# Kernel tuning notes

Hardware: AMD Instinct MI355X
Metric: run time of the kernel (lower is better)

Reference implementation:

```python
import jax, jax.numpy as jnp
import numpy as np

EPS = 1e-12
SMOOTH = 9.0
SGR_STEPS = 3


def l2norm(x, axis=-1):
    return x / jnp.maximum(jnp.linalg.norm(x, axis=axis, keepdims=True), EPS)


def setup_inputs() -> dict:
    key = jax.random.key(0)
    d, s = 1024, 256
    n_img, n_cap, L, n_tok = 64, 64, 32, 197  # 197 -> CLS + 14x14 grid

    def xavier(k, shape):
        lim = float(np.sqrt(6.0 / (shape[-2] + shape[-1])))
        return jax.random.uniform(k, shape, jnp.float32, -lim, lim)

    ks = iter(jax.random.split(key, 32))
    inp = {
        "img_embs": jax.random.normal(next(ks), (n_img, n_tok, d), jnp.float32),
        "cap_embs": jax.random.normal(next(ks), (n_cap, L, d), jnp.float32),
        # constant lengths == max length so the vectorized reference matches
        # the original per-caption loop exactly
        "cap_lens": jnp.full((n_cap,), L, dtype=jnp.int32),
        # visual GlobalSelfAttention
        "vG_Wl": xavier(next(ks), (d, d)), "vG_bl": jnp.zeros((d,), jnp.float32),
        "vG_Wg": xavier(next(ks), (d, d)), "vG_bg": jnp.zeros((d,), jnp.float32),
        "vG_Wc": xavier(next(ks), (d, 1)), "vG_bc": jnp.zeros((1,), jnp.float32),
        # textual GlobalSelfAttention
        "tG_Wl": xavier(next(ks), (d, d)), "tG_bl": jnp.zeros((d,), jnp.float32),
        "tG_Wg": xavier(next(ks), (d, d)), "tG_bg": jnp.zeros((d,), jnp.float32),
        "tG_Wc": xavier(next(ks), (d, 1)), "tG_bc": jnp.zeros((1,), jnp.float32),
        # similarity projections
        "W_loc": xavier(next(ks), (d, s)), "b_loc": jnp.zeros((s,), jnp.float32),
        "W_glo": xavier(next(ks), (d, s)), "b_glo": jnp.zeros((s,), jnp.float32),
        "W_eval": xavier(next(ks), (s, 1)), "b_eval": jnp.zeros((1,), jnp.float32),
        # 3 stacked GraphReasoning layers
        "sgr_Wq": xavier(next(ks), (SGR_STEPS, s, s)), "sgr_bq": jnp.zeros((SGR_STEPS, s), jnp.float32),
        "sgr_Wk": xavier(next(ks), (SGR_STEPS, s, s)), "sgr_bk": jnp.zeros((SGR_STEPS, s), jnp.float32),
        "sgr_Wg": xavier(next(ks), (SGR_STEPS, s, s)), "sgr_bg": jnp.zeros((SGR_STEPS, s), jnp.float32),
    }
    return inp


def global_self_attention(local, raw_global, Wl, bl, Wg, bg, Wc, bc):
    # local: (B, N, d), raw_global: (B, d); dropout is identity at eval
    le = jnp.tanh(local @ Wl + bl)
    ge = jnp.tanh(raw_global @ Wg + bg)
    logits = ((le * ge[:, None, :]) @ Wc + bc)[..., 0]  # (B, N)
    weights = jax.nn.softmax(logits, axis=1)
    global_feat = jnp.sum(weights[..., None] * local, axis=1)
    return l2norm(global_feat, axis=-1)


def scan_attention(query, context, smooth=SMOOTH):
    # query: (B, Nq, d), context: (B, Nc, d)
    attn = jnp.einsum("bcd,bqd->bcq", context, query)
    attn = jax.nn.leaky_relu(attn, negative_slope=0.1)
    attn = l2norm(attn, axis=2)                    # normalize over query dim
    attn = jnp.swapaxes(attn, 1, 2)                # (B, Nq, Nc)
    attn = jax.nn.softmax(attn * smooth, axis=2)   # softmax over context
    weighted = jnp.einsum("bqc,bcd->bqd", attn, context)
    return l2norm(weighted, axis=-1)


def graph_reasoning(sim_emb, Wq, bq, Wk, bk, Wg, bg):
    q = sim_emb @ Wq + bq
    k = sim_emb @ Wk + bk
    edge = jax.nn.softmax(jnp.einsum("bnd,bmd->bnm", q, k), axis=-1)
    sgr = jnp.einsum("bnm,bmd->bnd", edge, sim_emb)
    return jax.nn.relu(sgr @ Wg + bg)


def reference(img_embs, cap_embs, cap_lens,
              vG_Wl, vG_bl, vG_Wg, vG_bg, vG_Wc, vG_bc,
              tG_Wl, tG_bl, tG_Wg, tG_bg, tG_Wc, tG_bc,
              W_loc, b_loc, W_glo, b_glo, W_eval, b_eval,
              sgr_Wq, sgr_bq, sgr_Wk, sgr_bk, sgr_Wg, sgr_bg):
    # 197 tokens -> strip CLS (has_cls_token is True)
    img_tokens = img_embs[:, 1:, :]                      # (n_img, 196, d)
    n_img = img_tokens.shape[0]
    img_avg = img_tokens.mean(axis=1)
    img_global = global_self_attention(img_tokens, img_avg,
                                       vG_Wl, vG_bl, vG_Wg, vG_bg, vG_Wc, vG_bc)

    def per_caption(cap_i):                              # cap_i: (L, d)
        L, d = cap_i.shape
        cap_e = jnp.broadcast_to(cap_i[None], (n_img, L, d))
        cap_avg = jnp.broadcast_to(cap_i.mean(axis=0)[None], (n_img, d))
        cap_global = global_self_attention(cap_e, cap_avg,
                                           tG_Wl, tG_bl, tG_Wg, tG_bg, tG_Wc, tG_bc)
        ctx = scan_attention(cap_e, img_tokens)          # (n_img, L, d)
        sim_loc = l2norm((ctx - cap_e) ** 2 @ W_loc + b_loc, axis=-1)
        sim_glo = l2norm((img_global - cap_global) ** 2 @ W_glo + b_glo, axis=-1)
        sim_emb = jnp.concatenate([sim_glo[:, None, :], sim_loc], axis=1)
        for t in range(SGR_STEPS):
            sim_emb = graph_reasoning(sim_emb, sgr_Wq[t], sgr_bq[t],
                                      sgr_Wk[t], sgr_bk[t], sgr_Wg[t], sgr_bg[t])
        return jax.nn.sigmoid(sim_emb[:, 0, :] @ W_eval + b_eval)[:, 0]  # (n_img,)

    sims = jax.vmap(per_caption)(cap_embs)               # (n_cap, n_img)
    return sims.T                                        # (n_img, n_cap)
```

## Files before the change

kernel.cpp:

```cpp
#include <hip/hip_runtime.h>
#include <hip/hip_bf16.h>
#include <math.h>

#define NI 64
#define NC 64
#define NTOK 197
#define TT 196
#define CL 32
#define DD 1024
#define SS 256
#define NN 33
#define EPSN 1e-12f
#define SMOOTHF 9.0f
#define TP 224

typedef __attribute__((ext_vector_type(8))) short bfrag;
typedef __attribute__((ext_vector_type(4))) float f32x4;
#define MFMA(a, b, c) __builtin_amdgcn_mfma_f32_16x16x32_bf16((a), (b), (c), 0, 0, 0)

#define OFF_ATTNT  0
#define OFF_WTILE  14848
#define OFF_WMAX   23552
#define OFF_NRMS   24064
#define OFF_QN     24192
#define OFF_RNQ    24704
#define OFF_SEA    0
#define OFF_EB     17424
#define OFF_R1     22176
#define OFF_WKQ    29088
#define OFF_VBUF   30112
#define SMEM_BYTES 31392

__device__ __forceinline__ float warp_reduce_sum64(float v) {
#pragma unroll
  for (int m = 32; m > 0; m >>= 1) v += __shfl_xor(v, m, 64);
  return v;
}
__device__ __forceinline__ unsigned short f2b(float f) {
  __hip_bfloat16 h = __float2bfloat16(f);
  return *reinterpret_cast<unsigned short*>(&h);
}
__device__ __forceinline__ float b2f(unsigned short u) {
  union { unsigned int i; float f; } v;
  v.i = ((unsigned int)u) << 16;
  return v.f;
}

__global__ void k_avg(const float* __restrict__ img, const float* __restrict__ cap,
                      float* __restrict__ img_avg, float* __restrict__ cap_avg) {
  int bid = blockIdx.x;
  int tid = threadIdx.x;
  if (bid < NI) {
    int b = bid;
    for (int d = tid; d < DD; d += 256) {
      float acc = 0.f;
      const float* p = img + ((size_t)b * NTOK + 1) * DD + d;
      for (int t = 0; t < TT; ++t) acc += p[(size_t)t * DD];
      img_avg[b * DD + d] = acc * (1.0f / TT);
    }
  } else {
    int c = bid - NI;
    for (int d = tid; d < DD; d += 256) {
      float acc = 0.f;
      const float* p = cap + (size_t)c * CL * DD + d;
      for (int t = 0; t < CL; ++t) acc += p[(size_t)t * DD];
      cap_avg[c * DD + d] = acc * (1.0f / CL);
    }
  }
}

__global__ void k_hvec(const float* __restrict__ avg, const float* __restrict__ Wg,
                       const float* __restrict__ bg, const float* __restrict__ Wc,
                       float* __restrict__ h) {
  __shared__ float av[DD];
  int b = blockIdx.x >> 2;
  int dc = blockIdx.x & 3;
  int tid = threadIdx.x;
  for (int i = tid; i < DD; i += 256) av[i] = avg[b * DD + i];
  __syncthreads();
  int d = dc * 256 + tid;
  float acc = 0.f;
  for (int k = 0; k < DD; k += 4) {
    float4 a4 = *(const float4*)&av[k];
    acc += a4.x * Wg[(size_t)(k + 0) * DD + d];
    acc += a4.y * Wg[(size_t)(k + 1) * DD + d];
    acc += a4.z * Wg[(size_t)(k + 2) * DD + d];
    acc += a4.w * Wg[(size_t)(k + 3) * DD + d];
  }
  h[b * DD + d] = tanhf(acc + bg[d]) * Wc[d];
}

__global__ void k_logits2(const unsigned short* __restrict__ Ai, const unsigned short* __restrict__ Wi,
                          const float* __restrict__ bli, const float* __restrict__ hi,
                          float* __restrict__ pi,
                          const unsigned short* __restrict__ Ac, const unsigned short* __restrict__ Wc2,
                          const float* __restrict__ blc, const float* __restrict__ hc,
                          float* __restrict__ pc) {
  int tid = threadIdx.x;
  int lane = tid & 63, w = tid >> 6;
  int lrow = lane & 15, lk = (lane >> 4) * 8, rsub = (lane >> 4) * 4;
  int bx = blockIdx.x;
  const unsigned short* Abf;
  const unsigned short* WT;
  const float* bl;
  const float* h;
  float* partial;
  int rb, rowsPerBatch;
  if (bx < 196) {
    Abf = Ai; WT = Wi; bl = bli; h = hi; partial = pi; rb = bx * 64; rowsPerBatch = TT;
  } else {
    Abf = Ac; WT = Wc2; bl = blc; h = hc; partial = pc; rb = (bx - 196) * 64; rowsPerBatch = CL;
  }
  int c0 = blockIdx.y * 64;
  const unsigned short* ap = Abf + (size_t)(rb + w * 16 + lrow) * DD;
  f32x4 acc[4] = {};
  for (int k0 = 0; k0 < DD; k0 += 32) {
    bfrag a = *(const bfrag*)(ap + k0 + lk);
#pragma unroll
    for (int i = 0; i < 4; ++i) {
      bfrag bb = *(const bfrag*)(WT + (size_t)(c0 + i * 16 + lrow) * DD + k0 + lk);
      acc[i] = MFMA(a, bb, acc[i]);
    }
  }
#pragma unroll
  for (int r = 0; r < 4; ++r) {
    int row = rb + w * 16 + rsub + r;
    int bb2 = row / rowsPerBatch;
    float s = 0.f;
#pragma unroll
    for (int i = 0; i < 4; ++i) {
      int col = c0 + i * 16 + lrow;
      s += tanhf(acc[i][r] + bl[col]) * h[bb2 * DD + col];
    }
    s += __shfl_xor(s, 1, 64);
    s += __shfl_xor(s, 2, 64);
    s += __shfl_xor(s, 4, 64);
    s += __shfl_xor(s, 8, 64);
    if (lrow == 0) partial[(size_t)row * 16 + blockIdx.y] = s;
  }
}

__global__ void k_finish2(const float* __restrict__ pi, const float* __restrict__ bci,
                          const float* __restrict__ Xi, long bsi, int Ri, float* __restrict__ oi,
                          const float* __restrict__ pc, const float* __restrict__ bcc,
                          const float* __restrict__ Xc, long bsc, int Rc, float* __restrict__ oc) {
  __shared__ float w[200];
  __shared__ float red[8];
  int bid = blockIdx.x, tid = threadIdx.x;
  const float* partial;
  const float* bc;
  const float* Xbase;
  long batchStride;
  int R, b;
  float* outG;
  if (bid < 64) {
    partial = pi; bc = bci; Xbase = Xi; batchStride = bsi; R = Ri; outG = oi; b = bid;
  } else {
    partial = pc; bc = bcc; Xbase = Xc; batchStride = bsc; R = Rc; outG = oc; b = bid - 64;
  }
  for (int t = tid; t < R; t += 256) {
    const float* pp = &partial[((size_t)b * R + t) * 16];
    float s = bc[0];
#pragma unroll
    for (int u = 0; u < 16; ++u) s += pp[u];
    w[t] = s;
  }
  __syncthreads();
  float m = -1e30f;
  for (int t = tid; t < R; t += 256) m = fmaxf(m, w[t]);
#pragma unroll
  for (int mm = 32; mm; mm >>= 1) m = fmaxf(m, __shfl_xor(m, mm, 64));
  if ((tid & 63) == 0) red[tid >> 6] = m;
  __syncthreads();
  m = fmaxf(fmaxf(red[0], red[1]), fmaxf(red[2], red[3]));
  __syncthreads();
  for (int t = tid; t < R; t += 256) w[t] = expf(w[t] - m);
  __syncthreads();
  const float* xb = Xbase + (size_t)b * batchStride;
  float acc[4];
  float ss = 0.f;
#pragma unroll
  for (int c4 = 0; c4 < 4; ++c4) {
    int d = tid + c4 * 256;
    float a = 0.f;
    for (int t = 0; t < R; ++t) a += w[t] * xb[(size_t)t * DD + d];
    acc[c4] = a;
    ss += a * a;
  }
  ss = warp_reduce_sum64(ss);
  if ((tid & 63) == 0) red[tid >> 6] = ss;
  __syncthreads();
  ss = red[0] + red[1] + red[2] + red[3];
  float rn = 1.0f / fmaxf(sqrtf(ss), EPSN);
#pragma unroll
  for (int c4 = 0; c4 < 4; ++c4) outG[(size_t)b * DD + tid + c4 * 256] = acc[c4] * rn;
}

__global__ void k_simglo(const float* __restrict__ ig, const float* __restrict__ cg,
                         const float* __restrict__ W, const float* __restrict__ bgl,
                         float* __restrict__ simglo) {
  __shared__ float a_lds[32][20];
  __shared__ float b_lds[32][260];
  int tid = threadIdx.x;
  int p0 = blockIdx.x * 16;
  int ty = tid >> 6, tx = tid & 63;
  int s_rr = tid >> 3, s_kq = tid & 7;
  float acc[4][4] = {};
  for (int k0 = 0; k0 < DD; k0 += 32) {
    float d2[4] = {};
    if (tid < 128) {
      int p = p0 + s_rr;
      int b = p >> 6, c = p & 63;
      float4 giv = *(const float4*)&ig[b * DD + k0 + s_kq * 4];
      float4 cgv = *(const float4*)&cg[c * DD + k0 + s_kq * 4];
      float dx = giv.x - cgv.x, dy = giv.y - cgv.y, dz = giv.z - cgv.z, dw = giv.w - cgv.w;
      d2[0] = dx * dx; d2[1] = dy * dy; d2[2] = dz * dz; d2[3] = dw * dw;
    }
    float4 wv[8];
#pragma unroll
    for (int u = 0; u < 8; ++u)
      wv[u] = *(const float4*)&W[(size_t)(k0 + s_rr) * SS + s_kq * 32 + u * 4];
    __syncthreads();
    if (tid < 128) {
#pragma unroll
      for (int u = 0; u < 4; ++u) a_lds[s_kq * 4 + u][s_rr] = d2[u];
    }
#pragma unroll
    for (int u = 0; u < 8; ++u)
      *(float4*)&b_lds[s_rr][s_kq * 32 + u * 4] = wv[u];
    __syncthreads();
#pragma unroll
    for (int kk = 0; kk < 32; ++kk) {
      float4 a4 = *(const float4*)&a_lds[kk][ty * 4];
      float4 b4 = *(const float4*)&b_lds[kk][tx * 4];
      float av[4] = {a4.x, a4.y, a4.z, a4.w};
      float bv[4] = {b4.x, b4.y, b4.z, b4.w};
#pragma unroll
      for (int i = 0; i < 4; ++i)
#pragma unroll
        for (int j = 0; j < 4; ++j) acc[i][j] += av[i] * bv[j];
    }
  }
#pragma unroll
  for (int i = 0; i < 4; ++i) {
    float v[4];
    float ssq = 0.f;
#pragma unroll
    for (int j = 0; j < 4; ++j) {
      v[j] = acc[i][j] + bgl[tx * 4 + j];
      ssq += v[j] * v[j];
    }
    ssq = warp_reduce_sum64(ssq);
    float rn = 1.0f / fmaxf(sqrtf(ssq), EPSN);
    int p = p0 + ty * 4 + i;
    *(float4*)&simglo[(size_t)p * SS + tx * 4] =
        make_float4(v[0] * rn, v[1] * rn, v[2] * rn, v[3] * rn);
  }
}

__global__ void k_mmatb(const float* __restrict__ Wa, const float* __restrict__ Wb,
                        unsigned short* __restrict__ M) {
  __shared__ float a_lds[32][68];
  __shared__ float b_lds[32][68];
  int tid = threadIdx.x;
  int t = blockIdx.x >> 4;
  int dt = (blockIdx.x >> 2) & 3, et = blockIdx.x & 3;
  int d0 = dt * 64, e0 = et * 64;
  const float* wq = Wa + (size_t)t * SS * SS;
  const float* wk = Wb + (size_t)t * SS * SS;
  int ty = tid >> 4, tx = tid & 15;
  int s_rr = tid >> 2, s_kq = tid & 3;
  float acc[4][4] = {};
  for (int j0 = 0; j0 < SS; j0 += 32) {
    float4 q0 = *(const float4*)&wq[(size_t)(d0 + s_rr) * SS + j0 + s_kq * 8];
    float4 q1 = *(const float4*)&wq[(size_t)(d0 + s_rr) * SS + j0 + s_kq * 8 + 4];
    float4 k0v = *(const float4*)&wk[(size_t)(e0 + s_rr) * SS + j0 + s_kq * 8];
    float4 k1v = *(const float4*)&wk[(size_t)(e0 + s_rr) * SS + j0 + s_kq * 8 + 4];
    __syncthreads();
    float qa[8] = {q0.x, q0.y, q0.z, q0.w, q1.x, q1.y, q1.z, q1.w};
    float ka[8] = {k0v.x, k0v.y, k0v.z, k0v.w, k1v.x, k1v.y, k1v.z, k1v.w};
#pragma unroll
    for (int u = 0; u < 8; ++u) {
      a_lds[s_kq * 8 + u][s_rr] = qa[u];
      b_lds[s_kq * 8 + u][s_rr] = ka[u];
    }
    __syncthreads();
#pragma unroll
    for (int kk = 0; kk < 32; ++kk) {
      float4 a4 = *(const float4*)&a_lds[kk][ty * 4];
      float4 b4 = *(const float4*)&b_lds[kk][tx * 4];
      float av[4] = {a4.x, a4.y, a4.z, a4.w};
      float bv[4] = {b4.x, b4.y, b4.z, b4.w};
#pragma unroll
      for (int i = 0; i < 4; ++i)
#pragma unroll
        for (int j = 0; j < 4; ++j) acc[i][j] += av[i] * bv[j];
    }
  }
#pragma unroll
  for (int i = 0; i < 4; ++i) {
    unsigned int lo = (unsigned int)f2b(acc[i][0]) | ((unsigned int)f2b(acc[i][1]) << 16);
    unsigned int hi = (unsigned int)f2b(acc[i][2]) | ((unsigned int)f2b(acc[i][3]) << 16);
    uint2 o = make_uint2(lo, hi);
    *(uint2*)(M + (size_t)t * SS * SS + (size_t)(d0 + ty * 4 + i) * SS + e0 + tx * 4) = o;
  }
}

__global__ void k_wkbq(const float* __restrict__ Wk, const float* __restrict__ bq,
                       float* __restrict__ out) {
  __shared__ float bv[SS];
  int t = blockIdx.x, tid = threadIdx.x;
  const float* wk = Wk + (size_t)t * SS * SS;
  bv[tid] = bq[t * SS + tid];
  __syncthreads();
  float acc = 0.f;
  for (int j = 0; j < SS; j += 4) {
    float4 wv = *(const float4*)&wk[(size_t)tid * SS + j];
    float4 b4 = *(const float4*)&bv[j];
    acc += wv.x * b4.x + wv.y * b4.y + wv.z * b4.z + wv.w * b4.w;
  }
  out[t * SS + tid] = acc;
}

__global__ void k_imgprep(const float* __restrict__ img, unsigned short* __restrict__ row_bf,
                          unsigned short* __restrict__ tr_bf) {
  __shared__ float t[32][33];
  int b = blockIdx.z;
  int t0 = blockIdx.y * 32, d0 = blockIdx.x * 32;
  int tx = threadIdx.x & 31, ty = threadIdx.x >> 5;
#pragma unroll
  for (int u = 0; u < 4; ++u) {
    int tt = t0 + ty + u * 8;
    float v = (tt < TT) ? img[((size_t)b * NTOK + 1 + tt) * DD + d0 + tx] : 0.f;
    t[ty + u * 8][tx] = v;
    if (tt < TT) row_bf[((size_t)b * TT + tt) * DD + d0 + tx] = f2b(v);
  }
  __syncthreads();
#pragma unroll
  for (int u = 0; u < 4; ++u)
    tr_bf[((size_t)b * DD + d0 + ty + u * 8) * TP + t0 + tx] = f2b(t[tx][ty + u * 8]);
}

__global__ void k_gram_mfma(const unsigned short* __restrict__ img_bf,
                            unsigned short* __restrict__ gram) {
  int tid = threadIdx.x;
  int lane = tid & 63, w = tid >> 6;
  int lrow = lane & 15, lk = (lane >> 4) * 8, rsub = (lane >> 4) * 4;
  int bimg = blockIdx.x;
  int rb = blockIdx.y * 64, cb = blockIdx.z * 64;
  const unsigned short* X = img_bf + (size_t)bimg * TT * DD;
  int ra = rb + w * 16 + lrow;
  if (ra > TT - 1) ra = TT - 1;
  f32x4 acc[4] = {};
  for (int k0 = 0; k0 < DD; k0 += 32) {
    bfrag a = *(const bfrag*)(X + (size_t)ra * DD + k0 + lk);
#pragma unroll
    for (int i = 0; i < 4; ++i) {
      int cc = cb + i * 16 + lrow;
      if (cc > TT - 1) cc = TT - 1;
      bfrag bb = *(const bfrag*)(X + (size_t)cc * DD + k0 + lk);
      acc[i] = MFMA(a, bb, acc[i]);
    }
  }
  unsigned short* Gp = gram + (size_t)bimg * 208 * TP;
#pragma unroll
  for (int i = 0; i < 4; ++i) {
    int cc = cb + i * 16 + lrow;
#pragma unroll
    for (int r = 0; r < 4; ++r) {
      int rr = rb + w * 16 + rsub + r;
      if (rr < 208 && cc < TP)
        Gp[(size_t)rr * TP + cc] = (rr < TT && cc < TT) ? f2b(acc[i][r]) : 0;
    }
  }
}

__global__ void k_castb(const float* __restrict__ s, unsigned short* __restrict__ d, int n4) {
  int i = blockIdx.x * 256 + threadIdx.x;
  if (i < n4) {
    float4 v = *(const float4*)(s + (size_t)i * 4);
    uint2 o;
    o.x = (unsigned int)f2b(v.x) | ((unsigned int)f2b(v.y) << 16);
    o.y = (unsigned int)f2b(v.z) | ((unsigned int)f2b(v.w) << 16);
    *(uint2*)(d + (size_t)i * 4) = o;
  }
}

__global__ void k_tcast(const float* __restrict__ src, unsigned short* __restrict__ dst,
                        int R, int C, long sB, long dB) {
  __shared__ float t[32][33];
  const float* s = src + (size_t)blockIdx.z * sB;
  unsigned short* d = dst + (size_t)blockIdx.z * dB;
  int r0 = blockIdx.y * 32, c0 = blockIdx.x * 32;
  int tx = threadIdx.x & 31, ty = threadIdx.x >> 5;
#pragma unroll
  for (int u = 0; u < 4; ++u)
    t[ty + u * 8][tx] = s[(size_t)(r0 + ty + u * 8) * C + c0 + tx];
  __syncthreads();
#pragma unroll
  for (int u = 0; u < 4; ++u)
    d[(size_t)(c0 + ty + u * 8) * R + r0 + tx] = f2b(t[tx][ty + u * 8]);
}

__global__ __launch_bounds__(256, 4) void k_pair(
    const float* __restrict__ b_loc, const float* __restrict__ simglo,
    const float* __restrict__ wkbq, const float* __restrict__ bg3,
    const float* __restrict__ W_eval, const float* __restrict__ b_eval,
    const unsigned short* __restrict__ cap_bf, const unsigned short* __restrict__ img_bf,
    const unsigned short* __restrict__ imgT_bf, const unsigned short* __restrict__ gram_bf,
    const unsigned short* __restrict__ wlocT_bf, const unsigned short* __restrict__ mt_bf,
    const unsigned short* __restrict__ wgT_bf, float* __restrict__ out) {
  extern __shared__ char smem[];

  int tid = threadIdx.x;
  int lane = tid & 63, w = tid >> 6;
  int lrow = lane & 15;
  int lk = (lane >> 4) * 8;
  int rsub = (lane >> 4) * 4;
  int p = blockIdx.x;
  int b = p >> 6, c = p & 63;
  const unsigned short* imgR = img_bf + (size_t)b * TT * DD;
  const unsigned short* capB = cap_bf + (size_t)c * CL * DD;
  char* attnT_b = smem + OFF_ATTNT;

  {
    f32x4 acc[4][2] = {};
    for (int k0 = 0; k0 < DD; k0 += 32) {
      bfrag bq0 = *(const bfrag*)(capB + (size_t)lrow * DD + k0 + lk);
      bfrag bq1 = *(const bfrag*)(capB + (size_t)(16 + lrow) * DD + k0 + lk);
#pragma unroll
      for (int i = 0; i < 4; ++i) {
        int tt = w + 4 * i;
        if (tt < 13) {
          int t = tt * 16 + lrow;
          bfrag a = {0, 0, 0, 0, 0, 0, 0, 0};
          if (t < TT) a = *(const bfrag*)(imgR + (size_t)t * DD + k0 + lk);
          acc[i][0] = MFMA(a, bq0, acc[i][0]);
          acc[i][1] = MFMA(a, bq1, acc[i][1]);
        }
      }
    }
    float mx0 = -1e30f, mx1 = -1e30f;
#pragma unroll
    for (int i = 0; i < 4; ++i) {
      int tt = w + 4 * i;
      if (tt < 13) {
#pragma unroll
        for (int r = 0; r < 4; ++r) {
          int t = tt * 16 + rsub + r;
          float v0 = acc[i][0][r];
          v0 = v0 < 0.f ? 0.1f * v0 : v0;
          float v1 = acc[i][1][r];
          v1 = v1 < 0.f ? 0.1f * v1 : v1;
          float s2 = v0 * v0 + v1 * v1;
          s2 += __shfl_xor(s2, 1, 64);
          s2 += __shfl_xor(s2, 2, 64);
          s2 += __shfl_xor(s2, 4, 64);
          s2 += __shfl_xor(s2, 8, 64);
          float rn = 1.0f / fmaxf(sqrtf(s2), EPSN);
          v0 *= rn;
          v1 *= rn;
          acc[i][0][r] = v0;
          acc[i][1][r] = v1;
          if (t < TT) {
            mx0 = fmaxf(mx0, v0);
            mx1 = fmaxf(mx1, v1);
          }
        }
      }
    }
    mx0 = fmaxf(mx0, __shfl_xor(mx0, 16, 64));
    mx0 = fmaxf(mx0, __shfl_xor(mx0, 32, 64));
    mx1 = fmaxf(mx1, __shfl_xor(mx1, 16, 64));
    mx1 = fmaxf(mx1, __shfl_xor(mx1, 32, 64));
    float* wmax = (float*)(smem + OFF_WMAX);
    if ((lane >> 4) == 0) {
      wmax[w * 32 + lrow] = mx0;
      wmax[w * 32 + 16 + lrow] = mx1;
    }
    __syncthreads();
    mx0 = fmaxf(fmaxf(wmax[lrow], wmax[32 + lrow]), fmaxf(wmax[64 + lrow], wmax[96 + lrow]));
    mx1 = fmaxf(fmaxf(wmax[16 + lrow], wmax[48 + lrow]),
                fmaxf(wmax[80 + lrow], wmax[112 + lrow]));
#pragma unroll
    for (int i = 0; i < 4; ++i) {
      int tt = w + 4 * i;
#pragma unroll
      for (int r = 0; r < 4; ++r) {
        int t = tt * 16 + rsub + r;
        if (t < TP) {
          unsigned short e0 = 0, e1 = 0;
          if (t < TT) {
            e0 = f2b(expf(SMOOTHF * (acc[i][0][r] - mx0)));
            e1 = f2b(expf(SMOOTHF * (acc[i][1][r] - mx1)));
          }
          *(unsigned short*)(attnT_b + lrow * 464 + t * 2) = e0;
          *(unsigned short*)(attnT_b + (16 + lrow) * 464 + t * 2) = e1;
        }
      }
    }
  }
  __syncthreads();

  {
    float* qn = (float*)(smem + OFF_QN);
    float* nrmS = (float*)(smem + OFF_NRMS);
    const unsigned short* gb = gram_bf + (size_t)b * 208 * TP;
    float part0 = 0.f, part1 = 0.f;
#pragma unroll
    for (int i = 0; i < 4; ++i) {
      int tt = w + 4 * i;
      if (tt < 13) {
        f32x4 y0 = {0.f, 0.f, 0.f, 0.f}, y1 = {0.f, 0.f, 0.f, 0.f};
        for (int t0 = 0; t0 < TP; t0 += 32) {
          bfrag a = *(const bfrag*)(gb + (size_t)(tt * 16 + lrow) * TP + t0 + lk);
          bfrag b0 = *(const bfrag*)(attnT_b + lrow * 464 + (t0 + lk) * 2);
          bfrag b1 = *(const bfrag*)(attnT_b + (16 + lrow) * 464 + (t0 + lk) * 2);
          y0 = MFMA(a, b0, y0);
          y1 = MFMA(a, b1, y1);
        }
#pragma unroll
        for (int r = 0; r < 4; ++r) {
          int t = tt * 16 + rsub + r;
          if (t < TT) {
            part0 += y0[r] * b2f(*(const unsigned short*)(attnT_b + lrow * 464 + t * 2));
            part1 += y1[r] * b2f(*(const unsigned short*)(attnT_b + (16 + lrow) * 464 + t * 2));
          }
        }
      }
    }
    part0 += __shfl_xor(part0, 16, 64);
    part0 += __shfl_xor(part0, 32, 64);
    part1 += __shfl_xor(part1, 16, 64);
    part1 += __shfl_xor(part1, 32, 64);
    if ((lane >> 4) == 0) {
      qn[w * 32 + lrow] = part0;
      qn[w * 32 + 16 + lrow] = part1;
    }
    __syncthreads();
    if (tid < 32)
      nrmS[tid] = 1.0f / fmaxf(sqrtf(qn[tid] + qn[32 + tid] + qn[64 + tid] + qn[96 + tid]), EPSN);
    __syncthreads();
  }

  f32x4 accW[2][4] = {};
  {
    char* wtile_b = smem + OFF_WTILE;
    float* nrmS = (float*)(smem + OFF_NRMS);
    float nrm0 = nrmS[lrow], nrm1 = nrmS[16 + lrow];
    for (int d0 = 0; d0 < DD; d0 += 128) {
#pragma unroll
      for (int i = 0; i < 2; ++i) {
        f32x4 c2[2] = {};
        int dt = w + 4 * i;
        const unsigned short* ib = imgT_bf + ((size_t)b * DD + d0 + dt * 16 + lrow) * TP;
        for (int t0 = 0; t0 < TP; t0 += 32) {
          bfrag b0 = *(const bfrag*)(attnT_b + lrow * 464 + (t0 + lk) * 2);
          bfrag b1 = *(const bfrag*)(attnT_b + (16 + lrow) * 464 + (t0 + lk) * 2);
          bfrag a = *(const bfrag*)(ib + t0 + lk);
          c2[0] = MFMA(a, b0, c2[0]);
          c2[1] = MFMA(a, b1, c2[1]);
        }
        if (i == 0) __syncthreads();
        int dl = dt * 16 + rsub;
#pragma unroll
        for (int qt = 0; qt < 2; ++qt) {
          int q = qt * 16 + lrow;
          uint2 cu = *(const uint2*)(capB + (size_t)q * DD + d0 + dl);
          float cf0 = b2f(cu.x & 0xffff), cf1 = b2f(cu.x >> 16);
          float cf2 = b2f(cu.y & 0xffff), cf3 = b2f(cu.y >> 16);
          float rn = qt ? nrm1 : nrm0;
          float v0 = c2[qt][0] * rn - cf0;
          float v1 = c2[qt][1] * rn - cf1;
          float v2 = c2[qt][2] * rn - cf2;
          float v3 = c2[qt][3] * rn - cf3;
          unsigned int lo = (unsigned int)f2b(v0 * v0) | ((unsigned int)f2b(v1 * v1) << 16);
          unsigned int hi = (unsigned int)f2b(v2 * v2) | ((unsigned int)f2b(v3 * v3) << 16);
          *(uint2*)(wtile_b + q * 272 + dl * 2) = make_uint2(lo, hi);
        }
      }
      __syncthreads();
      for (int kc = 0; kc < 4; ++kc) {
        bfrag a0 = *(const bfrag*)(wtile_b + lrow * 272 + (kc * 32 + lk) * 2);
        bfrag a1 = *(const bfrag*)(wtile_b + (16 + lrow) * 272 + (kc * 32 + lk) * 2);
#pragma unroll
        for (int sti = 0; sti < 4; ++sti) {
          int s = (w * 4 + sti) * 16 + lrow;
          bfrag bb = *(const bfrag*)(wlocT_bf + (size_t)s * DD + d0 + kc * 32 + lk);
          accW[0][sti] = MFMA(a0, bb, accW[0][sti]);
          accW[1][sti] = MFMA(a1, bb, accW[1][sti]);
        }
      }
    }
  }

  {
    char* seA_b = smem + OFF_SEA;
    float* qn = (float*)(smem + OFF_QN);
    float* rnq = (float*)(smem + OFF_RNQ);
    __syncthreads();
    float blv[4];
#pragma unroll
    for (int sti = 0; sti < 4; ++sti) blv[sti] = b_loc[(w * 4 + sti) * 16 + lrow];
    float ss[2][4];
#pragma unroll
    for (int qt = 0; qt < 2; ++qt)
#pragma unroll
      for (int r = 0; r < 4; ++r) {
        float s2 = 0.f;
#pragma unroll
        for (int sti = 0; sti < 4; ++sti) {
          float v = accW[qt][sti][r] + blv[sti];
          s2 += v * v;
        }
        s2 += __shfl_xor(s2, 1, 64);
        s2 += __shfl_xor(s2, 2, 64);
        s2 += __shfl_xor(s2, 4, 64);
        s2 += __shfl_xor(s2, 8, 64);
        ss[qt][r] = s2;
      }
    if (lrow == 0) {
#pragma unroll
      for (int qt = 0; qt < 2; ++qt)
#pragma unroll
        for (int r = 0; r < 4; ++r)
          qn[w * 32 + qt * 16 + rsub + r] = ss[qt][r];
    }
    __syncthreads();
    if (tid < 32)
      rnq[tid] = 1.0f / fmaxf(sqrtf(qn[tid] + qn[32 + tid] + qn[64 + tid] + qn[96 + tid]), EPSN);
    __syncthreads();
#pragma unroll
    for (int qt = 0; qt < 2; ++qt)
#pragma unroll
      for (int r = 0; r < 4; ++r) {
        int q = qt * 16 + rsub + r;
        float rn = rnq[q];
#pragma unroll
        for (int sti = 0; sti < 4; ++sti) {
          int s = (w * 4 + sti) * 16 + lrow;
          float v = (accW[qt][sti][r] + blv[sti]) * rn;
          *(unsigned short*)(seA_b + (1 + q) * 528 + s * 2) = f2b(v);
        }
      }
    if (tid < 64) {
      float4 g4 = *(const float4*)&simglo[(size_t)p * SS + tid * 4];
      unsigned int lo = (unsigned int)f2b(g4.x) | ((unsigned int)f2b(g4.y) << 16);
      unsigned int hi = (unsigned int)f2b(g4.z) | ((unsigned int)f2b(g4.w) << 16);
      *(uint2*)(seA_b + tid * 8) = make_uint2(lo, hi);
    }
    __syncthreads();
  }

  {
    char* seA_b = smem + OFF_SEA;
    char* Gc_b = smem + OFF_R1;
    char* XT_b = smem + OFF_R1;
    float* Ef = (float*)(smem + OFF_R1);
    char* Eb = smem + OFF_EB;
    float* wkq = (float*)(smem + OFF_WKQ);
    float* vbuf = (float*)(smem + OFF_VBUF);

    for (int step = 0; step < 3; ++step) {
      const unsigned short* mstep = mt_bf + (size_t)step * SS * SS;
      const unsigned short* wstep = wgT_bf + (size_t)step * SS * SS;
      wkq[tid] = wkbq[step * SS + tid];
      __syncthreads();
      if (tid < 132) {
        int m = tid >> 2, qq = tid & 3;
        float a = 0.f;
        for (int e = qq * 64; e < qq * 64 + 64; e += 2) {
          unsigned int u = *(const unsigned int*)(seA_b + m * 528 + e * 2);
          a += b2f(u & 0xffff) * wkq[e] + b2f(u >> 16) * wkq[e + 1];
        }
        a += __shfl_xor(a, 1, 64);
        a += __shfl_xor(a, 2, 64);
        if (qq == 0) vbuf[m] = a;
      }
      f32x4 aE[3] = {};
      for (int ec = 0; ec < 4; ++ec) {
        f32x4 aGc[3] = {};
        for (int kc = 0; kc < 8; ++kc) {
          int k = kc * 32 + lk;
          bfrag bb = *(const bfrag*)(mstep + (size_t)(ec * 64 + w * 16 + lrow) * SS + k);
#pragma unroll
          for (int mt = 0; mt < 3; ++mt) {
            bfrag af = *(const bfrag*)(seA_b + (mt * 16 + lrow) * 528 + k * 2);
            aGc[mt] = MFMA(af, bb, aGc[mt]);
          }
        }
        __syncthreads();
#pragma unroll
        for (int mt = 0; mt < 3; ++mt)
#pragma unroll
          for (int r = 0; r < 4; ++r)
            *(unsigned short*)(Gc_b + (mt * 16 + rsub + r) * 144 + (w * 16 + lrow) * 2) =
                f2b(aGc[mt][r]);
        __syncthreads();
#pragma unroll
        for (int kc = 0; kc < 2; ++kc) {
          int k = kc * 32 + lk;
#pragma unroll
          for (int ti = 0; ti < 3; ++ti) {
            int tile = w + ti * 4;
            if (tile < 9) {
              int mtE = tile / 3, ntE = tile - mtE * 3;
              bfrag ga = *(const bfrag*)(Gc_b + (mtE * 16 + lrow) * 144 + k * 2);
              bfrag sb = *(const bfrag*)(seA_b + (ntE * 16 + lrow) * 528 + (ec * 64 + k) * 2);
              aE[ti] = MFMA(ga, sb, aE[ti]);
            }
          }
        }
      }
      __syncthreads();
#pragma unroll
      for (int ti = 0; ti < 3; ++ti) {
        int tile = w + ti * 4;
        if (tile < 9) {
          int mtE = tile / 3, ntE = tile - mtE * 3;
          int n0 = mtE * 16 + rsub, m = ntE * 16 + lrow;
#pragma unroll
          for (int r = 0; r < 4; ++r)
            if (n0 + r < NN && m < NN) Ef[(n0 + r) * 34 + m] = aE[ti][r] + vbuf[m];
        }
      }
      __syncthreads();
      if (tid < NN) {
        float mx = -1e30f;
        for (int mm = 0; mm < NN; ++mm) mx = fmaxf(mx, Ef[tid * 34 + mm]);
        float sum = 0.f;
        for (int mm = 0; mm < NN; ++mm) {
          float e = expf(Ef[tid * 34 + mm] - mx);
          Ef[tid * 34 + mm] = e;
          sum += e;
        }
        float rs = 1.0f / sum;
        for (int mm = 0; mm < NN; ++mm) Ef[tid * 34 + mm] *= rs;
      }
      __syncthreads();
      for (int idx = tid; idx < 33 * 36; idx += 256) {
        int n = idx / 36, mp = (idx - n * 36) * 2;
        unsigned int lo = (mp < NN) ? (unsigned int)f2b(Ef[n * 34 + mp]) : 0u;
        unsigned int hi = (mp + 1 < NN) ? (unsigned int)f2b(Ef[n * 34 + mp + 1]) : 0u;
        *(unsigned int*)(Eb + n * 144 + mp * 2) = lo | (hi << 16);
      }
      __syncthreads();
      unsigned int oPk[4][3][2];
#pragma unroll
      for (int sc = 0; sc < 4; ++sc) {
        f32x4 aX[3] = {};
        for (int kc = 0; kc < 8; ++kc) {
          int k = kc * 32 + lk;
          bfrag bb = *(const bfrag*)(wstep + (size_t)(sc * 64 + w * 16 + lrow) * SS + k);
#pragma unroll
          for (int mt = 0; mt < 3; ++mt) {
            bfrag af = *(const bfrag*)(seA_b + (mt * 16 + lrow) * 528 + k * 2);
            aX[mt] = MFMA(af, bb, aX[mt]);
          }
        }
        __syncthreads();
#pragma unroll
        for (int mt = 0; mt < 3; ++mt) {
          unsigned int lo = (unsigned int)f2b(aX[mt][0]) | ((unsigned int)f2b(aX[mt][1]) << 16);
          unsigned int hi = (unsigned int)f2b(aX[mt][2]) | ((unsigned int)f2b(aX[mt][3]) << 16);
          *(uint2*)(XT_b + (w * 16 + lrow) * 144 + (mt * 16 + rsub) * 2) = make_uint2(lo, hi);
        }
        *(uint2*)(XT_b + (w * 16 + lrow) * 144 + (48 + rsub) * 2) = make_uint2(0, 0);
        __syncthreads();
        f32x4 aO[3] = {};
#pragma unroll
        for (int kc = 0; kc < 2; ++kc) {
          int k = kc * 32 + lk;
          bfrag xa = *(const bfrag*)(XT_b + (w * 16 + lrow) * 144 + k * 2);
#pragma unroll
          for (int nt = 0; nt < 3; ++nt) {
            bfrag eb = *(const bfrag*)(Eb + (nt * 16 + lrow) * 144 + k * 2);
            aO[nt] = MFMA(xa, eb, aO[nt]);
          }
        }
        float bga[4];
#pragma unroll
        for (int r = 0; r < 4; ++r) bga[r] = bg3[step * SS + sc * 64 + w * 16 + rsub + r];
#pragma unroll
        for (int nt = 0; nt < 3; ++nt) {
          float v0 = fmaxf(aO[nt][0] + bga[0], 0.f);
          float v1 = fmaxf(aO[nt][1] + bga[1], 0.f);
          float v2 = fmaxf(aO[nt][2] + bga[2], 0.f);
          float v3 = fmaxf(aO[nt][3] + bga[3], 0.f);
          oPk[sc][nt][0] = (unsigned int)f2b(v0) | ((unsigned int)f2b(v1) << 16);
          oPk[sc][nt][1] = (unsigned int)f2b(v2) | ((unsigned int)f2b(v3) << 16);
        }
      }
#pragma unroll
      for (int sc = 0; sc < 4; ++sc)
#pragma unroll
        for (int nt = 0; nt < 3; ++nt) {
          int n = nt * 16 + lrow;
          if (n < NN)
            *(uint2*)(seA_b + n * 528 + (sc * 64 + w * 16 + rsub) * 2) =
                make_uint2(oPk[sc][nt][0], oPk[sc][nt][1]);
        }
      __syncthreads();
    }
  }

  if (tid < 64) {
    const char* seA_b = smem + OFF_SEA;
    uint2 u = *(const uint2*)(seA_b + tid * 8);
    float4 w4 = *(const float4*)&W_eval[tid * 4];
    float s = b2f(u.x & 0xffff) * w4.x + b2f(u.x >> 16) * w4.y +
              b2f(u.y & 0xffff) * w4.z + b2f(u.y >> 16) * w4.w;
    s = warp_reduce_sum64(s);
    if (tid == 0) out[b * 64 + c] = 1.0f / (1.0f + expf(-(s + b_eval[0])));
  }
}

extern "C" void kernel_launch(void* const* d_in, const int* in_sizes, int n_in,
                              void* d_out, int out_size, void* d_ws, size_t ws_size,
                              hipStream_t stream) {
  (void)in_sizes; (void)n_in; (void)out_size; (void)ws_size;
  const float* img = (const float*)d_in[0];
  const float* cap = (const float*)d_in[1];
  const float* vG_Wl = (const float*)d_in[3];
  const float* vG_bl = (const float*)d_in[4];
  const float* vG_Wg = (const float*)d_in[5];
  const float* vG_bg = (const float*)d_in[6];
  const float* vG_Wc = (const float*)d_in[7];
  const float* vG_bc = (const float*)d_in[8];
  const float* tG_Wl = (const float*)d_in[9];
  const float* tG_bl = (const float*)d_in[10];
  const float* tG_Wg = (const float*)d_in[11];
  const float* tG_bg = (const float*)d_in[12];
  const float* tG_Wc = (const float*)d_in[13];
  const float* tG_bc = (const float*)d_in[14];
  const float* W_loc = (const float*)d_in[15];
  const float* b_loc = (const float*)d_in[16];
  const float* W_glo = (const float*)d_in[17];
  const float* b_glo = (const float*)d_in[18];
  const float* W_eval = (const float*)d_in[19];
  const float* b_eval = (const float*)d_in[20];
  const float* sgr_Wq = (const float*)d_in[21];
  const float* sgr_bq = (const float*)d_in[22];
  const float* sgr_Wk = (const float*)d_in[23];
  const float* sgr_Wg = (const float*)d_in[25];
  const float* sgr_bg = (const float*)d_in[26];
  float* out = (float*)d_out;
  float* ws = (float*)d_ws;
  float* img_avg = ws;
  float* cap_avg = ws + 65536;
  float* h_img = ws + 131072;
  float* h_cap = ws + 196608;
  float* part_img = ws + 262144;
  float* part_cap = ws + 462848;
  float* img_glob = ws + 495616;
  float* cap_glob = ws + 561152;
  float* simglo = ws + 626688;
  float* wkbqv = ws + 1675264;
  unsigned short* ub = (unsigned short*)(ws + 1676032);
  unsigned short* mt_bf = ub;
  unsigned short* wgT_bf = ub + 196608;
  unsigned short* wlocT_bf = ub + 393216;
  unsigned short* cap_bf = ub + 655360;
  unsigned short* gram_bf = ub + 2752512;
  unsigned short* imgT_bf = ub + 5734400;
  unsigned short* img_bf = ub + 20414464;
  unsigned short* wlT_v = ub + 33259520;
  unsigned short* wlT_t = ub + 34308096;

  k_avg<<<128, 256, 0, stream>>>(img, cap, img_avg, cap_avg);
  k_hvec<<<256, 256, 0, stream>>>(img_avg, vG_Wg, vG_bg, vG_Wc, h_img);
  k_hvec<<<256, 256, 0, stream>>>(cap_avg, tG_Wg, tG_bg, tG_Wc, h_cap);
  k_imgprep<<<dim3(32, 7, 64), 256, 0, stream>>>(img, img_bf, imgT_bf);
  k_castb<<<2048, 256, 0, stream>>>(cap, cap_bf, 524288);
  k_tcast<<<dim3(32, 32, 1), 256, 0, stream>>>(vG_Wl, wlT_v, 1024, 1024, 0, 0);
  k_tcast<<<dim3(32, 32, 1), 256, 0, stream>>>(tG_Wl, wlT_t, 1024, 1024, 0, 0);
  k_logits2<<<dim3(228, 16), 256, 0, stream>>>(img_bf, wlT_v, vG_bl, h_img, part_img,
                                               cap_bf, wlT_t, tG_bl, h_cap, part_cap);
  k_finish2<<<128, 256, 0, stream>>>(part_img, vG_bc, img + DD, (long)NTOK * DD, TT, img_glob,
                                     part_cap, tG_bc, cap, (long)CL * DD, CL, cap_glob);
  k_simglo<<<256, 256, 0, stream>>>(img_glob, cap_glob, W_glo, b_glo, simglo);
  k_mmatb<<<48, 256, 0, stream>>>(sgr_Wk, sgr_Wq, mt_bf);
  k_wkbq<<<3, 256, 0, stream>>>(sgr_Wk, sgr_bq, wkbqv);
  k_gram_mfma<<<dim3(64, 4, 4), 256, 0, stream>>>(img_bf, gram_bf);
  k_tcast<<<dim3(8, 8, 3), 256, 0, stream>>>(sgr_Wg, wgT_bf, 256, 256, 65536, 65536);
  k_tcast<<<dim3(8, 32, 1), 256, 0, stream>>>(W_loc, wlocT_bf, 1024, 256, 0, 0);
  hipFuncSetAttribute((const void*)k_pair, hipFuncAttributeMaxDynamicSharedMemorySize,
                      SMEM_BYTES);
  k_pair<<<4096, 256, SMEM_BYTES, stream>>>(b_loc, simglo, wkbqv, sgr_bg, W_eval, b_eval,
                                            cap_bf, img_bf, imgT_bf, gram_bf, wlocT_bf,
                                            mt_bf, wgT_bf, out);
}
```

Baseline: 1.815 ms.

## Merge small prep kernels, use MFMA for global similarity, swizzle pair block order

Combines the two hvec launches, the four transpose-cast launches (now also casting W_glo) and the wkbq kernel into single multi-role launches, cutting launch count. The global-similarity projection is rewritten to use bf16 MFMA with one block per image instead of fp32 FMA tiles. The main pair kernel remaps block IDs so concurrently running blocks cover different image/caption combinations, which may change cache locality. The bf16 rounding of the squared differences in sim_glo adds precision loss.

```diff
diff --git a/kernel.cpp b/kernel.cpp
--- a/kernel.cpp
+++ b/kernel.cpp
@@ -69,12 +69,25 @@
   }
 }
 
-__global__ void k_hvec(const float* __restrict__ avg, const float* __restrict__ Wg,
-                       const float* __restrict__ bg, const float* __restrict__ Wc,
-                       float* __restrict__ h) {
+__global__ void k_hvec2(const float* __restrict__ img_avg, const float* __restrict__ cap_avg,
+                        const float* __restrict__ vWg, const float* __restrict__ vbg,
+                        const float* __restrict__ vWc, const float* __restrict__ tWg,
+                        const float* __restrict__ tbg, const float* __restrict__ tWc,
+                        float* __restrict__ h_img, float* __restrict__ h_cap) {
   __shared__ float av[DD];
-  int b = blockIdx.x >> 2;
-  int dc = blockIdx.x & 3;
+  int bid = blockIdx.x;
+  const float* avg;
+  const float* Wg;
+  const float* bg;
+  const float* Wc;
+  float* h;
+  if (bid < 256) {
+    avg = img_avg; Wg = vWg; bg = vbg; Wc = vWc; h = h_img;
+  } else {
+    avg = cap_avg; Wg = tWg; bg = tbg; Wc = tWc; h = h_cap; bid -= 256;
+  }
+  int b = bid >> 2;
+  int dc = bid & 3;
   int tid = threadIdx.x;
   for (int i = tid; i < DD; i += 256) av[i] = avg[b * DD + i];
   __syncthreads();
@@ -196,73 +209,86 @@
   for (int c4 = 0; c4 < 4; ++c4) outG[(size_t)b * DD + tid + c4 * 256] = acc[c4] * rn;
 }
 
-__global__ void k_simglo(const float* __restrict__ ig, const float* __restrict__ cg,
-                         const float* __restrict__ W, const float* __restrict__ bgl,
-                         float* __restrict__ simglo) {
-  __shared__ float a_lds[32][20];
-  __shared__ float b_lds[32][260];
+__global__ void k_simglo_m(const float* __restrict__ ig, const float* __restrict__ cg,
+                           const unsigned short* __restrict__ wgloT,
+                           const float* __restrict__ bgl, float* __restrict__ simglo) {
+  __shared__ unsigned short aL[64 * 40];
   int tid = threadIdx.x;
-  int p0 = blockIdx.x * 16;
-  int ty = tid >> 6, tx = tid & 63;
-  int s_rr = tid >> 3, s_kq = tid & 7;
-  float acc[4][4] = {};
+  int lane = tid & 63, w = tid >> 6;
+  int lrow = lane & 15, lk = (lane >> 4) * 8, rsub = (lane >> 4) * 4;
+  int b = blockIdx.x;
+  int srow = tid >> 2, skq = tid & 3;
+  f32x4 acc[16] = {};
   for (int k0 = 0; k0 < DD; k0 += 32) {
-    float d2[4] = {};
-    if (tid < 128) {
-      int p = p0 + s_rr;
-      int b = p >> 6, c = p & 63;
-      float4 giv = *(const float4*)&ig[b * DD + k0 + s_kq * 4];
-      float4 cgv = *(const float4*)&cg[c * DD + k0 + s_kq * 4];
-      float dx = giv.x - cgv.x, dy = giv.y - cgv.y, dz = giv.z - cgv.z, dw = giv.w - cgv.w;
-      d2[0] = dx * dx; d2[1] = dy * dy; d2[2] = dz * dz; d2[3] = dw * dw;
-    }
-    float4 wv[8];
-#pragma unroll
-    for (int u = 0; u < 8; ++u)
-      wv[u] = *(const float4*)&W[(size_t)(k0 + s_rr) * SS + s_kq * 32 + u * 4];
-    __syncthreads();
-    if (tid < 128) {
-#pragma unroll
-      for (int u = 0; u < 4; ++u) a_lds[s_kq * 4 + u][s_rr] = d2[u];
-    }
-#pragma unroll
-    for (int u = 0; u < 8; ++u)
-      *(float4*)&b_lds[s_rr][s_kq * 32 + u * 4] = wv[u];
-    __syncthreads();
-#pragma unroll
-    for (int kk = 0; kk < 32; ++kk) {
-      float4 a4 = *(const float4*)&a_lds[kk][ty * 4];
-      float4 b4 = *(const float4*)&b_lds[kk][tx * 4];
-      float av[4] = {a4.x, a4.y, a4.z, a4.w};
-      float bv[4] = {b4.x, b4.y, b4.z, b4.w};
-#pragma unroll
-      for (int i = 0; i < 4; ++i)
-#pragma unroll
-        for (int j = 0; j < 4; ++j) acc[i][j] += av[i] * bv[j];
-    }
-  }
-#pragma unroll
-  for (int i = 0; i < 4; ++i) {
-    float v[4];
+    const float* ip = ig + (size_t)b * DD + k0 + skq * 8;
+    const float* cp = cg + (size_t)srow * DD + k0 + skq * 8;
+    float4 i0 = *(const float4*)ip;
+    float4 i1 = *(const float4*)(ip + 4);
+    float4 c0 = *(const float4*)cp;
+    float4 c1 = *(const float4*)(cp + 4);
+    float d0 = i0.x - c0.x, d1 = i0.y - c0.y, d2 = i0.z - c0.z, d3 = i0.w - c0.w;
+    float d4 = i1.x - c1.x, d5 = i1.y - c1.y, d6 = i1.z - c1.z, d7 = i1.w - c1.w;
+    uint4 o;
+    o.x = (unsigned int)f2b(d0 * d0) | ((unsigned int)f2b(d1 * d1) << 16);
+    o.y = (unsigned int)f2b(d2 * d2) | ((unsigned int)f2b(d3 * d3) << 16);
+    o.z = (unsigned int)f2b(d4 * d4) | ((unsigned int)f2b(d5 * d5) << 16);
+    o.w = (unsigned int)f2b(d6 * d6) | ((unsigned int)f2b(d7 * d7) << 16);
+    __syncthreads();
+    *(uint4*)&aL[srow * 40 + skq * 8] = o;
+    __syncthreads();
+    bfrag af = *(const bfrag*)&aL[(w * 16 + lrow) * 40 + lk];
+#pragma unroll
+    for (int ct = 0; ct < 16; ++ct) {
+      bfrag bb = *(const bfrag*)(wgloT + (size_t)(ct * 16 + lrow) * DD + k0 + lk);
+      acc[ct] = MFMA(af, bb, acc[ct]);
+    }
+  }
+  float bglv[16];
+#pragma unroll
+  for (int ct = 0; ct < 16; ++ct) bglv[ct] = bgl[ct * 16 + lrow];
+#pragma unroll
+  for (int r = 0; r < 4; ++r) {
+    int crow = w * 16 + rsub + r;
+    float vv[16];
     float ssq = 0.f;
 #pragma unroll
-    for (int j = 0; j < 4; ++j) {
-      v[j] = acc[i][j] + bgl[tx * 4 + j];
-      ssq += v[j] * v[j];
-    }
-    ssq = warp_reduce_sum64(ssq);
+    for (int ct = 0; ct < 16; ++ct) {
+      float v = acc[ct][r] + bglv[ct];
+      vv[ct] = v;
+      ssq += v * v;
+    }
+    ssq += __shfl_xor(ssq, 1, 64);
+    ssq += __shfl_xor(ssq, 2, 64);
+    ssq += __shfl_xor(ssq, 4, 64);
+    ssq += __shfl_xor(ssq, 8, 64);
     float rn = 1.0f / fmaxf(sqrtf(ssq), EPSN);
-    int p = p0 + ty * 4 + i;
-    *(float4*)&simglo[(size_t)p * SS + tx * 4] =
-        make_float4(v[0] * rn, v[1] * rn, v[2] * rn, v[3] * rn);
+    float* op = simglo + ((size_t)b * 64 + crow) * SS;
+#pragma unroll
+    for (int ct = 0; ct < 16; ++ct) op[ct * 16 + lrow] = vv[ct] * rn;
   }
 }
 
 __global__ void k_mmatb(const float* __restrict__ Wa, const float* __restrict__ Wb,
-                        unsigned short* __restrict__ M) {
+                        unsigned short* __restrict__ M, const float* __restrict__ bq,
+                        float* __restrict__ wkbqv) {
   __shared__ float a_lds[32][68];
   __shared__ float b_lds[32][68];
+  __shared__ float bv[SS];
   int tid = threadIdx.x;
+  if (blockIdx.x >= 48) {
+    int t = blockIdx.x - 48;
+    const float* wk = Wb + (size_t)t * SS * SS;
+    bv[tid] = bq[t * SS + tid];
+    __syncthreads();
+    float acc = 0.f;
+    for (int j = 0; j < SS; j += 4) {
+      float4 wv = *(const float4*)&wk[(size_t)tid * SS + j];
+      float4 b4 = *(const float4*)&bv[j];
+      acc += wv.x * b4.x + wv.y * b4.y + wv.z * b4.z + wv.w * b4.w;
+    }
+    wkbqv[t * SS + tid] = acc;
+    return;
+  }
   int t = blockIdx.x >> 4;
   int dt = (blockIdx.x >> 2) & 3, et = blockIdx.x & 3;
   int d0 = dt * 64, e0 = et * 64;
@@ -290,11 +316,11 @@
       float4 a4 = *(const float4*)&a_lds[kk][ty * 4];
       float4 b4 = *(const float4*)&b_lds[kk][tx * 4];
       float av[4] = {a4.x, a4.y, a4.z, a4.w};
-      float bv[4] = {b4.x, b4.y, b4.z, b4.w};
+      float bvv[4] = {b4.x, b4.y, b4.z, b4.w};
 #pragma unroll
       for (int i = 0; i < 4; ++i)
 #pragma unroll
-        for (int j = 0; j < 4; ++j) acc[i][j] += av[i] * bv[j];
+        for (int j = 0; j < 4; ++j) acc[i][j] += av[i] * bvv[j];
     }
   }
 #pragma unroll
@@ -304,22 +330,6 @@
     uint2 o = make_uint2(lo, hi);
     *(uint2*)(M + (size_t)t * SS * SS + (size_t)(d0 + ty * 4 + i) * SS + e0 + tx * 4) = o;
   }
-}
-
-__global__ void k_wkbq(const float* __restrict__ Wk, const float* __restrict__ bq,
-                       float* __restrict__ out) {
-  __shared__ float bv[SS];
-  int t = blockIdx.x, tid = threadIdx.x;
-  const float* wk = Wk + (size_t)t * SS * SS;
-  bv[tid] = bq[t * SS + tid];
-  __syncthreads();
-  float acc = 0.f;
-  for (int j = 0; j < SS; j += 4) {
-    float4 wv = *(const float4*)&wk[(size_t)tid * SS + j];
-    float4 b4 = *(const float4*)&bv[j];
-    acc += wv.x * b4.x + wv.y * b4.y + wv.z * b4.z + wv.w * b4.w;
-  }
-  out[t * SS + tid] = acc;
 }
 
 __global__ void k_imgprep(const float* __restrict__ img, unsigned short* __restrict__ row_bf,
@@ -386,12 +396,32 @@
   }
 }
 
-__global__ void k_tcast(const float* __restrict__ src, unsigned short* __restrict__ dst,
-                        int R, int C, long sB, long dB) {
+__global__ void k_tcast_all(const float* __restrict__ vWl, const float* __restrict__ tWl,
+                            const float* __restrict__ sWg, const float* __restrict__ Wloc,
+                            const float* __restrict__ Wglo,
+                            unsigned short* __restrict__ wlT_v, unsigned short* __restrict__ wlT_t,
+                            unsigned short* __restrict__ wgT3, unsigned short* __restrict__ wlocT,
+                            unsigned short* __restrict__ wgloT) {
   __shared__ float t[32][33];
-  const float* s = src + (size_t)blockIdx.z * sB;
-  unsigned short* d = dst + (size_t)blockIdx.z * dB;
-  int r0 = blockIdx.y * 32, c0 = blockIdx.x * 32;
+  int id = blockIdx.x;
+  const float* s;
+  unsigned short* d;
+  int R, C;
+  if (id < 1024) {
+    s = vWl; d = wlT_v; R = 1024; C = 1024;
+  } else if (id < 2048) {
+    s = tWl; d = wlT_t; R = 1024; C = 1024; id -= 1024;
+  } else if (id < 2240) {
+    id -= 2048;
+    int tb = id >> 6; id &= 63;
+    s = sWg + (size_t)tb * 65536; d = wgT3 + (size_t)tb * 65536; R = 256; C = 256;
+  } else if (id < 2496) {
+    s = Wloc; d = wlocT; R = 1024; C = 256; id -= 2240;
+  } else {
+    s = Wglo; d = wgloT; R = 1024; C = 256; id -= 2496;
+  }
+  int ct = C >> 5;
+  int r0 = (id / ct) * 32, c0 = (id % ct) * 32;
   int tx = threadIdx.x & 31, ty = threadIdx.x >> 5;
 #pragma unroll
   for (int u = 0; u < 4; ++u)
@@ -417,7 +447,7 @@
   int lrow = lane & 15;
   int lk = (lane >> 4) * 8;
   int rsub = (lane >> 4) * 4;
-  int p = blockIdx.x;
+  int p = ((blockIdx.x & 7) << 9) | (blockIdx.x >> 3);
   int b = p >> 6, c = p & 63;
   const unsigned short* imgR = img_bf + (size_t)b * TT * DD;
   const unsigned short* capB = cap_bf + (size_t)c * CL * DD;
@@ -866,24 +896,22 @@
   unsigned short* img_bf = ub + 20414464;
   unsigned short* wlT_v = ub + 33259520;
   unsigned short* wlT_t = ub + 34308096;
+  unsigned short* wgloT = ub + 35356672;
 
   k_avg<<<128, 256, 0, stream>>>(img, cap, img_avg, cap_avg);
-  k_hvec<<<256, 256, 0, stream>>>(img_avg, vG_Wg, vG_bg, vG_Wc, h_img);
-  k_hvec<<<256, 256, 0, stream>>>(cap_avg, tG_Wg, tG_bg, tG_Wc, h_cap);
   k_imgprep<<<dim3(32, 7, 64), 256, 0, stream>>>(img, img_bf, imgT_bf);
   k_castb<<<2048, 256, 0, stream>>>(cap, cap_bf, 524288);
-  k_tcast<<<dim3(32, 32, 1), 256, 0, stream>>>(vG_Wl, wlT_v, 1024, 1024, 0, 0);
-  k_tcast<<<dim3(32, 32, 1), 256, 0, stream>>>(tG_Wl, wlT_t, 1024, 1024, 0, 0);
+  k_tcast_all<<<2752, 256, 0, stream>>>(vG_Wl, tG_Wl, sgr_Wg, W_loc, W_glo,
+                                        wlT_v, wlT_t, wgT_bf, wlocT_bf, wgloT);
+  k_hvec2<<<512, 256, 0, stream>>>(img_avg, cap_avg, vG_Wg, vG_bg, vG_Wc,
+                                   tG_Wg, tG_bg, tG_Wc, h_img, h_cap);
   k_logits2<<<dim3(228, 16), 256, 0, stream>>>(img_bf, wlT_v, vG_bl, h_img, part_img,
                                                cap_bf, wlT_t, tG_bl, h_cap, part_cap);
   k_finish2<<<128, 256, 0, stream>>>(part_img, vG_bc, img + DD, (long)NTOK * DD, TT, img_glob,
                                      part_cap, tG_bc, cap, (long)CL * DD, CL, cap_glob);
-  k_simglo<<<256, 256, 0, stream>>>(img_glob, cap_glob, W_glo, b_glo, simglo);
-  k_mmatb<<<48, 256, 0, stream>>>(sgr_Wk, sgr_Wq, mt_bf);
-  k_wkbq<<<3, 256, 0, stream>>>(sgr_Wk, sgr_bq, wkbqv);
+  k_simglo_m<<<64, 256, 0, stream>>>(img_glob, cap_glob, wgloT, b_glo, simglo);
+  k_mmatb<<<51, 256, 0, stream>>>(sgr_Wk, sgr_Wq, mt_bf, sgr_bq, wkbqv);
   k_gram_mfma<<<dim3(64, 4, 4), 256, 0, stream>>>(img_bf, gram_bf);
-  k_tcast<<<dim3(8, 8, 3), 256, 0, stream>>>(sgr_Wg, wgT_bf, 256, 256, 65536, 65536);
-  k_tcast<<<dim3(8, 32, 1), 256, 0, stream>>>(W_loc, wlocT_bf, 1024, 256, 0, 0);
   hipFuncSetAttribute((const void*)k_pair, hipFuncAttributeMaxDynamicSharedMemorySize,
                       SMEM_BYTES);
   k_pair<<<4096, 256, SMEM_BYTES, stream>>>(b_loc, simglo, wkbqv, sgr_bg, W_eval, b_eval,
```

Result: faster. 1.717 ms (-5.4%).
